# Kernel optimization log

Hardware: AMD Instinct MI355X
Metric: run time of the kernel (lower is better)

The kernel has to match this reference:

```python
import jax, jax.numpy as jnp
import numpy as np

K = 20        # knn neighbors (hardcoded default in get_graph_feature)
EPS = 1e-5    # BatchNorm eps (torch default)


def _bn(x, gamma, beta):
    # training-mode BatchNorm2d: batch stats over (B, N, k) per channel; x: (B, C, N, k)
    mean = jnp.mean(x, axis=(0, 2, 3), keepdims=True)
    var = jnp.var(x, axis=(0, 2, 3), keepdims=True)  # biased, as torch uses for normalization
    return (x - mean) * jax.lax.rsqrt(var + EPS) * gamma[None, :, None, None] + beta[None, :, None, None]


def _graph_feature(x, k):
    # x: (B, D, N) -> (B, 2D, N, k)  [edge features: (neighbor, center)]
    xt = jnp.swapaxes(x, 1, 2)                       # (B, N, D)
    sq = jnp.sum(x * x, axis=1)                      # (B, N)
    inner = jnp.einsum('bnd,bmd->bnm', xt, xt)       # (B, N, N)
    neg_dist = 2.0 * inner - sq[:, :, None] - sq[:, None, :]  # -||xi-xj||^2
    _, idx = jax.lax.top_k(neg_dist, k)              # (B, N, k) nearest neighbors
    feat = jax.vmap(lambda f, i: f[i])(xt, idx)      # (B, N, k, D) gather
    center = jnp.broadcast_to(xt[:, :, None, :], feat.shape)
    g = jnp.concatenate([feat, center], axis=-1)     # (B, N, k, 2D)
    return jnp.transpose(g, (0, 3, 1, 2))            # (B, 2D, N, k)


def _conv1x1(W, x):
    # W: (out, in), x: (B, in, N, k)
    return jnp.einsum('oi,bink->bonk', W, x)


def setup_inputs() -> dict:
    key = jax.random.key(0)
    ks = jax.random.split(key, 16)
    B, D, N = 8, 3, 2048
    emb = 512
    points = jax.random.normal(ks[0], (B, D, N), dtype=jnp.float32)

    def w(k, o, i):
        return jax.random.normal(k, (o, i), dtype=jnp.float32) * (1.0 / np.sqrt(i))

    inp = {
        'points': points,
        'W1': w(ks[1], 64, 6),
        'W2': w(ks[2], 64, 64),
        'W3': w(ks[3], 128, 64),
        'W4': w(ks[4], 256, 128),
        'W5': w(ks[5], emb, 512),
    }
    chans = [64, 64, 128, 256, emb]
    for j, c in enumerate(chans):
        inp[f'g{j+1}'] = 1.0 + 0.1 * jax.random.normal(ks[6 + j], (c,), dtype=jnp.float32)
        inp[f'b{j+1}'] = 0.1 * jax.random.normal(ks[11 + j], (c,), dtype=jnp.float32)
    return inp


def reference(points, W1, W2, W3, W4, W5, g1, b1, g2, b2, g3, b3, g4, b4, g5, b5):
    B, D, N = points.shape
    x = points - jnp.mean(points, axis=2, keepdims=True)   # de-mean (equivariant embedding)
    h = _graph_feature(x, K)                                # (B, 6, N, K)
    h = jax.nn.relu(_bn(_conv1x1(W1, h), g1, b1))
    x1 = jnp.max(h, axis=-1, keepdims=True)                 # (B, 64, N, 1)
    h = jax.nn.relu(_bn(_conv1x1(W2, h), g2, b2))
    x2 = jnp.max(h, axis=-1, keepdims=True)                 # (B, 64, N, 1)
    h = jax.nn.relu(_bn(_conv1x1(W3, h), g3, b3))
    x3 = jnp.max(h, axis=-1, keepdims=True)                 # (B, 128, N, 1)
    h = jax.nn.relu(_bn(_conv1x1(W4, h), g4, b4))
    x4 = jnp.max(h, axis=-1, keepdims=True)                 # (B, 256, N, 1)
    xc = jnp.concatenate([x1, x2, x3, x4], axis=1)          # (B, 512, N, 1)
    out = _bn(_conv1x1(W5, xc), g5, b5).reshape(B, -1, N)   # (B, emb, N)
    return jax.nn.relu(out)
```

## Files before the change

### kernel.cpp

```cpp
#include <hip/hip_runtime.h>

#define BB 8
#define NN 2048
#define KNN 20
#define NPOS (BB*NN)
#define NEDGE (NPOS*KNN)

typedef _Float16 f16x8 __attribute__((ext_vector_type(8)));
typedef float f32x4 __attribute__((ext_vector_type(4)));

union H16 { _Float16 h; unsigned short u; };
__device__ __forceinline__ unsigned short f2h(float f){ H16 x; x.h = (_Float16)f; return x.u; }
__device__ __forceinline__ float h2f(unsigned short u){ H16 x; x.u = u; return (float)x.h; }
__device__ __forceinline__ unsigned fmap(float f){ unsigned u = __float_as_uint(f); return (u & 0x80000000u) ? ~u : (u | 0x80000000u); }
__device__ __forceinline__ float funmap(unsigned m){ return __uint_as_float((m & 0x80000000u) ? (m & 0x7fffffffu) : ~m); }

__global__ __launch_bounds__(256) void k_demean(const float* __restrict__ pts, float* __restrict__ xt){
  int b = blockIdx.x / 3, d = blockIdx.x % 3;
  const float* row = pts + (size_t)(b*3 + d)*NN;
  __shared__ float red[256];
  int t = threadIdx.x;
  float s = 0.f;
  for (int n = t; n < NN; n += 256) s += row[n];
  red[t] = s; __syncthreads();
  for (int w = 128; w > 0; w >>= 1){ if (t < w) red[t] += red[t+w]; __syncthreads(); }
  float mean = red[0] * (1.0f/NN);
  for (int n = t; n < NN; n += 256) xt[(size_t)(b*NN + n)*4 + d] = row[n] - mean;
}

__global__ __launch_bounds__(256) void k_knn(const float* __restrict__ xt, unsigned short* __restrict__ idxo){
  __shared__ float4 xl[NN];
  __shared__ float tv[KNN][256];
  __shared__ unsigned short ti[KNN][256];
  int b = blockIdx.x >> 6;
  int pbase = (blockIdx.x & 63) * 32;
  int t = threadIdx.x;
  const float4* xb = (const float4*)xt + (size_t)b*NN;
  for (int m = t; m < NN; m += 256){
    float4 v = xb[m];
    v.w = v.x*v.x + v.y*v.y + v.z*v.z;
    xl[m] = v;
  }
  __syncthreads();
  int pl = t >> 3, g = t & 7;
  int n = pbase + pl;
  float4 xn = xl[n];
  float sqn = xn.w;
  for (int j = 0; j < 20; ++j){
    int m = g + (j << 3);
    float4 xm = xl[m];
    float nd = 2.f*(xn.x*xm.x + xn.y*xm.y + xn.z*xm.z) - sqn - xm.w;
    tv[j][t] = nd; ti[j][t] = (unsigned short)m;
  }
  float curmin = tv[0][t]; int minslot = 0;
  #pragma unroll
  for (int j = 1; j < 20; ++j){ float v = tv[j][t]; if (v < curmin){ curmin = v; minslot = j; } }
  for (int j = 20; j < 256; ++j){
    int m = g + (j << 3);
    float4 xm = xl[m];
    float nd = 2.f*(xn.x*xm.x + xn.y*xm.y + xn.z*xm.z) - sqn - xm.w;
    if (nd > curmin){
      tv[minslot][t] = nd; ti[minslot][t] = (unsigned short)m;
      curmin = tv[0][t]; minslot = 0;
      #pragma unroll
      for (int u = 1; u < 20; ++u){ float vv = tv[u][t]; if (vv < curmin){ curmin = vv; minslot = u; } }
    }
  }
  __syncthreads();
  for (int s = 4; s; s >>= 1){
    if (g < s){
      int src = t + s;
      for (int jj = 0; jj < 20; ++jj){
        float v = tv[jj][src];
        if (v > curmin){
          unsigned short mi = ti[jj][src];
          tv[minslot][t] = v; ti[minslot][t] = mi;
          curmin = tv[0][t]; minslot = 0;
          #pragma unroll
          for (int u = 1; u < 20; ++u){ float vv = tv[u][t]; if (vv < curmin){ curmin = vv; minslot = u; } }
        }
      }
    }
    __syncthreads();
  }
  if (g == 0){
    unsigned short* op = idxo + (size_t)(b*NN + pbase + pl)*KNN;
    #pragma unroll
    for (int j = 0; j < 20; ++j) op[j] = ti[j][t];
  }
}

__global__ __launch_bounds__(256) void k_conv1(const float* __restrict__ xt, const unsigned short* __restrict__ idx,
    const float* __restrict__ W1, unsigned short* __restrict__ y1){
  __shared__ float Wl[64*6];
  int t = threadIdx.x;
  for (int i = t; i < 384; i += 256) Wl[i] = W1[i];
  __syncthreads();
  int e = blockIdx.x*256 + t;
  int p = e / KNN;
  int b = p >> 11;
  int n = p & (NN-1);
  int nb = idx[e];
  const float4* xb = (const float4*)xt + (size_t)b*NN;
  float4 xnb = xb[nb], xcn = xb[n];
  unsigned short* yo = y1 + (size_t)e*64;
  #pragma unroll
  for (int o = 0; o < 64; o += 8){
    unsigned short pk[8];
    #pragma unroll
    for (int q = 0; q < 8; ++q){
      const float* w = &Wl[(o+q)*6];
      float v = w[0]*xnb.x + w[1]*xnb.y + w[2]*xnb.z + w[3]*xcn.x + w[4]*xcn.y + w[5]*xcn.z;
      pk[q] = f2h(v);
    }
    uint4 u;
    u.x = (unsigned)pk[0] | ((unsigned)pk[1]<<16);
    u.y = (unsigned)pk[2] | ((unsigned)pk[3]<<16);
    u.z = (unsigned)pk[4] | ((unsigned)pk[5]<<16);
    u.w = (unsigned)pk[6] | ((unsigned)pk[7]<<16);
    *reinterpret_cast<uint4*>(yo + o) = u;
  }
}

__global__ __launch_bounds__(256) void k_stats1(const unsigned short* __restrict__ y, float* __restrict__ st){
  int t = threadIdx.x;
  int c = t & 63, ro = t >> 6;
  float s = 0.f, q = 0.f;
  for (int rb = blockIdx.x; rb < NEDGE/4; rb += gridDim.x){
    float v = h2f(y[(size_t)(rb*4 + ro)*64 + c]);
    s += v; q += v*v;
  }
  __shared__ float red[256];
  red[t] = s; __syncthreads();
  if (t < 64){ for (int g = 1; g < 4; ++g) s += red[t + g*64]; }
  __syncthreads(); red[t] = q; __syncthreads();
  if (t < 64){
    for (int g = 1; g < 4; ++g) q += red[t + g*64];
    int shard = blockIdx.x & 63;
    atomicAdd(&st[c*64 + shard], s);
    atomicAdd(&st[64*64 + c*64 + shard], q);
  }
}

__global__ void k_fin(const float* __restrict__ st, const float* __restrict__ gw, const float* __restrict__ bw,
                      float* __restrict__ act, int C, float inv_n){
  int c = threadIdx.x;
  if (c >= C) return;
  float s = 0.f, q = 0.f;
  for (int i = 0; i < 64; ++i){ s += st[c*64 + i]; q += st[(size_t)C*64 + c*64 + i]; }
  float mean = s*inv_n;
  float var = q*inv_n - mean*mean;
  float sc = gw[c] * rsqrtf(var + 1e-5f);
  act[2*c] = sc; act[2*c+1] = bw[c] - mean*sc;
}

__global__ __launch_bounds__(256) void k_max64(const unsigned short* __restrict__ y, const float* __restrict__ actp,
    unsigned short* __restrict__ xc, int xcoff){
  int gidx = blockIdx.x*256 + threadIdx.x;
  int q = gidx >> 5, cp = gidx & 31;
  int c = cp*2;
  float sc0 = actp[2*c],   sh0 = actp[2*c+1];
  float sc1 = actp[2*c+2], sh1 = actp[2*c+3];
  const unsigned* base = reinterpret_cast<const unsigned*>(y + (size_t)q*KNN*64 + c);
  float m0 = 0.f, m1 = 0.f;
  #pragma unroll
  for (int j = 0; j < KNN; ++j){
    unsigned v = base[(size_t)j*32];
    m0 = fmaxf(m0, sc0*h2f((unsigned short)(v & 0xffffu)) + sh0);
    m1 = fmaxf(m1, sc1*h2f((unsigned short)(v >> 16)) + sh1);
  }
  unsigned outv = (unsigned)f2h(m0) | ((unsigned)f2h(m1) << 16);
  *reinterpret_cast<unsigned*>(xc + (size_t)q*512 + xcoff + c) = outv;
}

__device__ __forceinline__ int tix(int row, int col){ return row*64 + (col ^ ((row & 7) << 2)); }

template<int CIN, int COUT, bool ACT, bool MINMAX, bool BGLOBAL, bool SPLITIN>
__global__ __launch_bounds__(256) void k_mfma(
    const unsigned short* __restrict__ inA, const unsigned short* __restrict__ inB,
    const float* __restrict__ W, const float* __restrict__ actp,
    unsigned short* __restrict__ out, size_t slab_stride,
    float* __restrict__ stat, unsigned* __restrict__ mx, unsigned* __restrict__ mn,
    int ntiles){
  constexpr int NKC = CIN/32;
  __shared__ __align__(16) float T[128*64];
  int t = threadIdx.x, lane = t & 63, w = t >> 6, g = lane >> 4, r16 = lane & 15;
  int o0 = blockIdx.y * 64;
  const f16x8 zf = 0;

  f16x8 breg[BGLOBAL ? 1 : NKC][4];
  if constexpr (!BGLOBAL){
    #pragma unroll
    for (int kc = 0; kc < NKC; ++kc)
      #pragma unroll
      for (int n = 0; n < 4; ++n){
        const float* wp = W + (size_t)(o0 + 16*n + r16)*CIN + kc*32 + g*8;
        float4 w0 = *reinterpret_cast<const float4*>(wp);
        float4 w1 = *reinterpret_cast<const float4*>(wp + 4);
        f16x8 bv;
        bv[0]=(_Float16)w0.x; bv[1]=(_Float16)w0.y; bv[2]=(_Float16)w0.z; bv[3]=(_Float16)w0.w;
        bv[4]=(_Float16)w1.x; bv[5]=(_Float16)w1.y; bv[6]=(_Float16)w1.z; bv[7]=(_Float16)w1.w;
        breg[kc][n] = bv;
      }
  }
  f16x8 scl8[ACT ? NKC : 1], shf8[ACT ? NKC : 1];
  if constexpr (ACT){
    #pragma unroll
    for (int kc = 0; kc < NKC; ++kc){
      int ch0 = kc*32 + g*8;
      const float4* apv = reinterpret_cast<const float4*>(actp + 2*ch0);
      float4 q0 = apv[0], q1 = apv[1], q2 = apv[2], q3 = apv[3];
      f16x8 s, h;
      s[0]=(_Float16)q0.x; h[0]=(_Float16)q0.y; s[1]=(_Float16)q0.z; h[1]=(_Float16)q0.w;
      s[2]=(_Float16)q1.x; h[2]=(_Float16)q1.y; s[3]=(_Float16)q1.z; h[3]=(_Float16)q1.w;
      s[4]=(_Float16)q2.x; h[4]=(_Float16)q2.y; s[5]=(_Float16)q2.z; h[5]=(_Float16)q2.w;
      s[6]=(_Float16)q3.x; h[6]=(_Float16)q3.y; s[7]=(_Float16)q3.z; h[7]=(_Float16)q3.w;
      scl8[kc] = s; shf8[kc] = h;
    }
  }
  float sAcc = 0.f, qAcc = 0.f;
  int cst = t & 63, ps = t >> 6;

  for (int tt = blockIdx.x; tt < ntiles; tt += gridDim.x){
    int p0 = tt * 128;
    int prow = p0 + 32*w + r16;
    f32x4 acc[2][4];
    #pragma unroll
    for (int m = 0; m < 2; ++m)
      #pragma unroll
      for (int n = 0; n < 4; ++n) acc[m][n] = 0.f;

    #pragma unroll
    for (int kc = 0; kc < NKC; ++kc){
      f16x8 af[2];
      #pragma unroll
      for (int m = 0; m < 2; ++m){
        const unsigned short* abase; int kloc, stride;
        if constexpr (SPLITIN){ abase = (kc < NKC/2) ? inA : inB; kloc = kc & (NKC/2 - 1); stride = 64; }
        else { abase = inA; kloc = kc; stride = CIN; }
        f16x8 av = *reinterpret_cast<const f16x8*>(abase + (size_t)(prow + 16*m)*stride + kloc*32 + g*8);
        if constexpr (ACT){
          av = av * scl8[kc] + shf8[kc];
          av = __builtin_elementwise_max(av, zf);
        }
        af[m] = av;
      }
      #pragma unroll
      for (int n = 0; n < 4; ++n){
        f16x8 bv;
        if constexpr (BGLOBAL){
          const float* wp = W + (size_t)(o0 + 16*n + r16)*CIN + kc*32 + g*8;
          float4 w0 = *reinterpret_cast<const float4*>(wp);
          float4 w1 = *reinterpret_cast<const float4*>(wp + 4);
          bv[0]=(_Float16)w0.x; bv[1]=(_Float16)w0.y; bv[2]=(_Float16)w0.z; bv[3]=(_Float16)w0.w;
          bv[4]=(_Float16)w1.x; bv[5]=(_Float16)w1.y; bv[6]=(_Float16)w1.z; bv[7]=(_Float16)w1.w;
        } else bv = breg[kc][n];
        acc[0][n] = __builtin_amdgcn_mfma_f32_16x16x32_f16(af[0], bv, acc[0][n], 0, 0, 0);
        acc[1][n] = __builtin_amdgcn_mfma_f32_16x16x32_f16(af[1], bv, acc[1][n], 0, 0, 0);
      }
    }
    __syncthreads();
    #pragma unroll
    for (int m = 0; m < 2; ++m)
      #pragma unroll
      for (int n = 0; n < 4; ++n)
        #pragma unroll
        for (int r = 0; r < 4; ++r)
          T[tix(32*w + 16*m + 4*g + r, 16*n + r16)] = acc[m][n][r];
    __syncthreads();
    #pragma unroll
    for (int r = 0; r < 32; ++r){
      float v = T[tix(32*ps + r, cst)];
      sAcc += v; qAcc += v*v;
    }
    if constexpr (!MINMAX){
      int row = t >> 1, h = t & 1;
      unsigned short* op = out + (size_t)blockIdx.y*slab_stride + ((size_t)p0 + row)*64 + 32*h;
      unsigned pk[16];
      #pragma unroll
      for (int i = 0; i < 8; ++i){
        float4 v = *reinterpret_cast<const float4*>(&T[tix(row, 32*h + 4*i)]);
        pk[2*i]   = (unsigned)f2h(v.x) | ((unsigned)f2h(v.y) << 16);
        pk[2*i+1] = (unsigned)f2h(v.z) | ((unsigned)f2h(v.w) << 16);
      }
      #pragma unroll
      for (int j = 0; j < 4; ++j){
        uint4 u; u.x = pk[4*j]; u.y = pk[4*j+1]; u.z = pk[4*j+2]; u.w = pk[4*j+3];
        *reinterpret_cast<uint4*>(op + 8*j) = u;
      }
    } else {
      int rlo = p0 + 32*ps, rhi = rlo + 32;
      for (int q = rlo/KNN; q*KNN < rhi; ++q){
        int lo = q*KNN > rlo ? q*KNN : rlo;
        int hi = (q*KNN + KNN) < rhi ? (q*KNN + KNN) : rhi;
        float mxv = -1e30f, mnv = 1e30f;
        for (int r = lo; r < hi; ++r){
          float v = T[tix(r - p0, cst)];
          mxv = fmaxf(mxv, v); mnv = fminf(mnv, v);
        }
        atomicMax(&mx[(size_t)q*COUT + o0 + cst], fmap(mxv));
        atomicMin(&mn[(size_t)q*COUT + o0 + cst], fmap(mnv));
      }
    }
  }
  __syncthreads();
  T[ps*64 + cst] = sAcc;
  __syncthreads();
  float stot = 0.f;
  if (t < 64) stot = T[t] + T[64+t] + T[128+t] + T[192+t];
  __syncthreads();
  T[ps*64 + cst] = qAcc;
  __syncthreads();
  if (t < 64){
    float qtot = T[t] + T[64+t] + T[128+t] + T[192+t];
    int shard = blockIdx.x & 63;
    atomicAdd(&stat[(size_t)(o0 + t)*64 + shard], stot);
    atomicAdd(&stat[(size_t)COUT*64 + (size_t)(o0 + t)*64 + shard], qtot);
  }
}

__global__ __launch_bounds__(256) void k_pool4(const unsigned* __restrict__ mx, const unsigned* __restrict__ mn,
    const float* __restrict__ actp, unsigned short* __restrict__ xc){
  int gidx = blockIdx.x*256 + threadIdx.x;
  int q = gidx >> 8, c = gidx & 255;
  float sc = actp[2*c], sh = actp[2*c+1];
  float raw = (sc >= 0.f) ? funmap(mx[gidx]) : funmap(mn[gidx]);
  xc[(size_t)q*512 + 256 + c] = f2h(fmaxf(0.f, sc*raw + sh));
}

__global__ void k_out(const unsigned short* __restrict__ y5, const float* __restrict__ actp, float* __restrict__ out){
  __shared__ float tile[32][33];
  int b = blockIdx.z, n0 = blockIdx.x*32, c0 = blockIdx.y*32;
  int lx = threadIdx.x, ly = threadIdx.y;
  int slab = c0 >> 6, cin = (c0 & 63) + lx;
  float sc = actp[2*(c0+lx)], sh = actp[2*(c0+lx)+1];
  const unsigned short* yb = y5 + (size_t)slab*NPOS*64 + (size_t)(b*NN + n0)*64 + cin;
  for (int yy = ly; yy < 32; yy += 8)
    tile[yy][lx] = fmaxf(0.f, sc*h2f(yb[(size_t)yy*64]) + sh);
  __syncthreads();
  for (int yy = ly; yy < 32; yy += 8)
    out[((size_t)(b*512 + c0 + yy))*NN + n0 + lx] = tile[lx][yy];
}

extern "C" void kernel_launch(void* const* d_in, const int* in_sizes, int n_in,
                              void* d_out, int out_size, void* d_ws, size_t ws_size,
                              hipStream_t stream){
  const float* pts = (const float*)d_in[0];
  const float* W1 = (const float*)d_in[1];
  const float* W2 = (const float*)d_in[2];
  const float* W3 = (const float*)d_in[3];
  const float* W4 = (const float*)d_in[4];
  const float* W5 = (const float*)d_in[5];
  const float* g1 = (const float*)d_in[6];  const float* b1 = (const float*)d_in[7];
  const float* g2 = (const float*)d_in[8];  const float* b2 = (const float*)d_in[9];
  const float* g3 = (const float*)d_in[10]; const float* b3 = (const float*)d_in[11];
  const float* g4 = (const float*)d_in[12]; const float* b4 = (const float*)d_in[13];
  const float* g5 = (const float*)d_in[14]; const float* b5 = (const float*)d_in[15];

  char* ws = (char*)d_ws;
  float*          xt    = (float*)(ws + 0);
  unsigned short* idxu  = (unsigned short*)(ws + 262144);
  float*          stats = (float*)(ws + 917504);
  float*          acts  = (float*)(ws + 1441792);
  unsigned short* y1    = (unsigned short*)(ws + 2097152);
  unsigned short* y3a   = (unsigned short*)(ws + 2097152);
  unsigned short* y5    = (unsigned short*)(ws + 2097152);
  unsigned short* y2    = (unsigned short*)(ws + 44040192);
  unsigned*       mx    = (unsigned*)(ws + 44040192);
  unsigned*       mn    = (unsigned*)(ws + 60817408);
  unsigned short* y3b   = (unsigned short*)(ws + 85983232);
  unsigned short* xc    = (unsigned short*)(ws + 127926272);
  float* out = (float*)d_out;

  float* st1 = stats + 0,  *st2 = stats + 8192, *st3 = stats + 16384, *st4 = stats + 32768, *st5 = stats + 65536;
  float* ac1 = acts + 0,   *ac2 = acts + 128,   *ac3 = acts + 256,    *ac4 = acts + 512,    *ac5 = acts + 1024;
  const size_t y3stride = (size_t)(85983232 - 2097152) / 2;

  hipMemsetAsync(stats, 0, 524288, stream);
  k_demean<<<24, 256, 0, stream>>>(pts, xt);
  k_knn<<<512, 256, 0, stream>>>(xt, idxu);
  k_conv1<<<NEDGE/256, 256, 0, stream>>>(xt, idxu, W1, y1);
  k_stats1<<<256, 256, 0, stream>>>(y1, st1);
  k_fin<<<1, 64, 0, stream>>>(st1, g1, b1, ac1, 64, 1.f/NEDGE);
  k_max64<<<NPOS*32/256, 256, 0, stream>>>(y1, ac1, xc, 0);
  k_mfma<64,64,true,false,false,false><<<dim3(1280,1), 256, 0, stream>>>(
      y1, nullptr, W2, ac1, y2, 0, st2, nullptr, nullptr, 2560);
  k_fin<<<1, 64, 0, stream>>>(st2, g2, b2, ac2, 64, 1.f/NEDGE);
  k_max64<<<NPOS*32/256, 256, 0, stream>>>(y2, ac2, xc, 64);
  k_mfma<64,128,true,false,false,false><<<dim3(640,2), 256, 0, stream>>>(
      y2, nullptr, W3, ac2, y3a, y3stride, st3, nullptr, nullptr, 2560);
  k_fin<<<1, 128, 0, stream>>>(st3, g3, b3, ac3, 128, 1.f/NEDGE);
  k_max64<<<NPOS*32/256, 256, 0, stream>>>(y3a, ac3, xc, 128);
  k_max64<<<NPOS*32/256, 256, 0, stream>>>(y3b, ac3 + 128, xc, 192);
  hipMemsetAsync(mx, 0x00, 16777216, stream);
  hipMemsetAsync(mn, 0xFF, 16777216, stream);
  k_mfma<128,256,true,true,false,true><<<dim3(320,4), 256, 0, stream>>>(
      y3a, y3b, W4, ac3, nullptr, 0, st4, mx, mn, 2560);
  k_fin<<<1, 256, 0, stream>>>(st4, g4, b4, ac4, 256, 1.f/NEDGE);
  k_pool4<<<NPOS, 256, 0, stream>>>(mx, mn, ac4, xc);
  k_mfma<512,512,false,false,true,false><<<dim3(128,8), 256, 0, stream>>>(
      xc, nullptr, W5, nullptr, y5, (size_t)NPOS*64, st5, nullptr, nullptr, 128);
  k_fin<<<1, 512, 0, stream>>>(st5, g5, b5, ac5, 512, 1.f/NPOS);
  k_out<<<dim3(NN/32, 16, BB), dim3(32, 8), 0, stream>>>(y5, ac5, out);
}
```

Measured before the change: 662.0 us.

## Restructure conv layers: per-wave point-aligned MFMA tiles with fused min/max pooling

```diff
diff --git a/kernel.cpp b/kernel.cpp
--- a/kernel.cpp
+++ b/kernel.cpp
@@ -7,13 +7,15 @@
 #define NEDGE (NPOS*KNN)
 
 typedef _Float16 f16x8 __attribute__((ext_vector_type(8)));
+typedef __fp16 fp16x2 __attribute__((ext_vector_type(2)));
 typedef float f32x4 __attribute__((ext_vector_type(4)));
 
 union H16 { _Float16 h; unsigned short u; };
 __device__ __forceinline__ unsigned short f2h(float f){ H16 x; x.h = (_Float16)f; return x.u; }
 __device__ __forceinline__ float h2f(unsigned short u){ H16 x; x.u = u; return (float)x.h; }
-__device__ __forceinline__ unsigned fmap(float f){ unsigned u = __float_as_uint(f); return (u & 0x80000000u) ? ~u : (u | 0x80000000u); }
-__device__ __forceinline__ float funmap(unsigned m){ return __uint_as_float((m & 0x80000000u) ? (m & 0x7fffffffu) : ~m); }
+__device__ __forceinline__ unsigned pkrtz(float a, float b){
+  union { fp16x2 h; unsigned u; } c; c.h = __builtin_amdgcn_cvt_pkrtz(a, b); return c.u;
+}
 
 __global__ __launch_bounds__(256) void k_demean(const float* __restrict__ pts, float* __restrict__ xt){
   int b = blockIdx.x / 3, d = blockIdx.x % 3;
@@ -88,6 +90,17 @@
     #pragma unroll
     for (int j = 0; j < 20; ++j) op[j] = ti[j][t];
   }
+}
+
+__global__ __launch_bounds__(256) void k_wprep(const float* __restrict__ W2, const float* __restrict__ W3,
+    const float* __restrict__ W4, const float* __restrict__ W5, unsigned short* __restrict__ wh){
+  int i = blockIdx.x*256 + threadIdx.x;
+  float v;
+  if (i < 4096) v = W2[i];
+  else if (i < 12288) v = W3[i-4096];
+  else if (i < 45056) v = W4[i-12288];
+  else v = W5[i-45056];
+  wh[i] = f2h(v);
 }
 
 __global__ __launch_bounds__(256) void k_conv1(const float* __restrict__ xt, const unsigned short* __restrict__ idx,
@@ -106,18 +119,16 @@
   unsigned short* yo = y1 + (size_t)e*64;
   #pragma unroll
   for (int o = 0; o < 64; o += 8){
-    unsigned short pk[8];
-    #pragma unroll
-    for (int q = 0; q < 8; ++q){
-      const float* w = &Wl[(o+q)*6];
-      float v = w[0]*xnb.x + w[1]*xnb.y + w[2]*xnb.z + w[3]*xcn.x + w[4]*xcn.y + w[5]*xcn.z;
-      pk[q] = f2h(v);
-    }
-    uint4 u;
-    u.x = (unsigned)pk[0] | ((unsigned)pk[1]<<16);
-    u.y = (unsigned)pk[2] | ((unsigned)pk[3]<<16);
-    u.z = (unsigned)pk[4] | ((unsigned)pk[5]<<16);
-    u.w = (unsigned)pk[6] | ((unsigned)pk[7]<<16);
+    unsigned pk[4];
+    #pragma unroll
+    for (int q = 0; q < 4; ++q){
+      const float* wa = &Wl[(o+2*q)*6];
+      const float* wb = &Wl[(o+2*q+1)*6];
+      float va = wa[0]*xnb.x + wa[1]*xnb.y + wa[2]*xnb.z + wa[3]*xcn.x + wa[4]*xcn.y + wa[5]*xcn.z;
+      float vb = wb[0]*xnb.x + wb[1]*xnb.y + wb[2]*xnb.z + wb[3]*xcn.x + wb[4]*xcn.y + wb[5]*xcn.z;
+      pk[q] = pkrtz(va, vb);
+    }
+    uint4 u; u.x = pk[0]; u.y = pk[1]; u.z = pk[2]; u.w = pk[3];
     *reinterpret_cast<uint4*>(yo + o) = u;
   }
 }
@@ -169,46 +180,25 @@
     m0 = fmaxf(m0, sc0*h2f((unsigned short)(v & 0xffffu)) + sh0);
     m1 = fmaxf(m1, sc1*h2f((unsigned short)(v >> 16)) + sh1);
   }
-  unsigned outv = (unsigned)f2h(m0) | ((unsigned)f2h(m1) << 16);
-  *reinterpret_cast<unsigned*>(xc + (size_t)q*512 + xcoff + c) = outv;
-}
-
-__device__ __forceinline__ int tix(int row, int col){ return row*64 + (col ^ ((row & 7) << 2)); }
-
-template<int CIN, int COUT, bool ACT, bool MINMAX, bool BGLOBAL, bool SPLITIN>
-__global__ __launch_bounds__(256) void k_mfma(
-    const unsigned short* __restrict__ inA, const unsigned short* __restrict__ inB,
-    const float* __restrict__ W, const float* __restrict__ actp,
-    unsigned short* __restrict__ out, size_t slab_stride,
-    float* __restrict__ stat, unsigned* __restrict__ mx, unsigned* __restrict__ mn,
-    int ntiles){
+  *reinterpret_cast<unsigned*>(xc + (size_t)q*512 + xcoff + c) = pkrtz(m0, m1);
+}
+
+template<int CIN, int COUT, bool ACT, bool POOL>
+__global__ __launch_bounds__(256, 4) void k_cstore(
+    const unsigned short* __restrict__ in, const unsigned short* __restrict__ Wh,
+    const float* __restrict__ actp, unsigned short* __restrict__ out, size_t slabStride,
+    float* __restrict__ stat, unsigned* __restrict__ pm, int Cpm, int NT){
   constexpr int NKC = CIN/32;
-  __shared__ __align__(16) float T[128*64];
-  int t = threadIdx.x, lane = t & 63, w = t >> 6, g = lane >> 4, r16 = lane & 15;
+  __shared__ unsigned short Tw[4][32][68];
+  int t = threadIdx.x, lane = t & 63, w = t >> 6;
+  int g = lane >> 4, r16 = lane & 15;
   int o0 = blockIdx.y * 64;
-  const f16x8 zf = 0;
-
-  f16x8 breg[BGLOBAL ? 1 : NKC][4];
-  if constexpr (!BGLOBAL){
-    #pragma unroll
-    for (int kc = 0; kc < NKC; ++kc)
-      #pragma unroll
-      for (int n = 0; n < 4; ++n){
-        const float* wp = W + (size_t)(o0 + 16*n + r16)*CIN + kc*32 + g*8;
-        float4 w0 = *reinterpret_cast<const float4*>(wp);
-        float4 w1 = *reinterpret_cast<const float4*>(wp + 4);
-        f16x8 bv;
-        bv[0]=(_Float16)w0.x; bv[1]=(_Float16)w0.y; bv[2]=(_Float16)w0.z; bv[3]=(_Float16)w0.w;
-        bv[4]=(_Float16)w1.x; bv[5]=(_Float16)w1.y; bv[6]=(_Float16)w1.z; bv[7]=(_Float16)w1.w;
-        breg[kc][n] = bv;
-      }
-  }
+  const f16x8 zf = (f16x8)(_Float16)0.f;
   f16x8 scl8[ACT ? NKC : 1], shf8[ACT ? NKC : 1];
   if constexpr (ACT){
     #pragma unroll
     for (int kc = 0; kc < NKC; ++kc){
-      int ch0 = kc*32 + g*8;
-      const float4* apv = reinterpret_cast<const float4*>(actp + 2*ch0);
+      const float4* apv = reinterpret_cast<const float4*>(actp + 2*(kc*32 + g*8));
       float4 q0 = apv[0], q1 = apv[1], q2 = apv[2], q3 = apv[3];
       f16x8 s, h;
       s[0]=(_Float16)q0.x; h[0]=(_Float16)q0.y; s[1]=(_Float16)q0.z; h[1]=(_Float16)q0.w;
@@ -218,114 +208,206 @@
       scl8[kc] = s; shf8[kc] = h;
     }
   }
-  float sAcc = 0.f, qAcc = 0.f;
-  int cst = t & 63, ps = t >> 6;
-
-  for (int tt = blockIdx.x; tt < ntiles; tt += gridDim.x){
-    int p0 = tt * 128;
-    int prow = p0 + 32*w + r16;
+  float sA[4][4] = {}, qA[4][4] = {};
+  int wid = blockIdx.x*4 + w;
+  for (int tt = wid; tt < NT; tt += gridDim.x*4){
+    int p0 = POOL ? tt*20 : tt*32;
+    int ra = p0 + r16, rb = p0 + 16 + r16;
+    if constexpr (POOL){ ra = min(ra, NEDGE-1); rb = min(rb, NEDGE-1); }
     f32x4 acc[2][4];
     #pragma unroll
     for (int m = 0; m < 2; ++m)
       #pragma unroll
       for (int n = 0; n < 4; ++n) acc[m][n] = 0.f;
-
-    #pragma unroll
+    #pragma unroll 4
     for (int kc = 0; kc < NKC; ++kc){
-      f16x8 af[2];
-      #pragma unroll
-      for (int m = 0; m < 2; ++m){
-        const unsigned short* abase; int kloc, stride;
-        if constexpr (SPLITIN){ abase = (kc < NKC/2) ? inA : inB; kloc = kc & (NKC/2 - 1); stride = 64; }
-        else { abase = inA; kloc = kc; stride = CIN; }
-        f16x8 av = *reinterpret_cast<const f16x8*>(abase + (size_t)(prow + 16*m)*stride + kloc*32 + g*8);
-        if constexpr (ACT){
-          av = av * scl8[kc] + shf8[kc];
-          av = __builtin_elementwise_max(av, zf);
+      f16x8 a0 = *reinterpret_cast<const f16x8*>(in + (size_t)ra*CIN + kc*32 + g*8);
+      f16x8 a1 = *reinterpret_cast<const f16x8*>(in + (size_t)rb*CIN + kc*32 + g*8);
+      if constexpr (ACT){
+        a0 = __builtin_elementwise_max(a0*scl8[kc] + shf8[kc], zf);
+        a1 = __builtin_elementwise_max(a1*scl8[kc] + shf8[kc], zf);
+      }
+      #pragma unroll
+      for (int n = 0; n < 4; ++n){
+        f16x8 bv = *reinterpret_cast<const f16x8*>(Wh + (size_t)(o0 + 16*n + r16)*CIN + kc*32 + g*8);
+        acc[0][n] = __builtin_amdgcn_mfma_f32_16x16x32_f16(bv, a0, acc[0][n], 0, 0, 0);
+        acc[1][n] = __builtin_amdgcn_mfma_f32_16x16x32_f16(bv, a1, acc[1][n], 0, 0, 0);
+      }
+    }
+    #pragma unroll
+    for (int n = 0; n < 4; ++n)
+      #pragma unroll
+      for (int r = 0; r < 4; ++r){
+        float v0 = acc[0][n][r];
+        sA[n][r] += v0; qA[n][r] += v0*v0;
+        if (!POOL || r16 < 4){
+          float v1 = acc[1][n][r];
+          sA[n][r] += v1; qA[n][r] += v1*v1;
         }
-        af[m] = av;
-      }
+      }
+    #pragma unroll
+    for (int m = 0; m < 2; ++m)
       #pragma unroll
       for (int n = 0; n < 4; ++n){
-        f16x8 bv;
-        if constexpr (BGLOBAL){
-          const float* wp = W + (size_t)(o0 + 16*n + r16)*CIN + kc*32 + g*8;
-          float4 w0 = *reinterpret_cast<const float4*>(wp);
-          float4 w1 = *reinterpret_cast<const float4*>(wp + 4);
-          bv[0]=(_Float16)w0.x; bv[1]=(_Float16)w0.y; bv[2]=(_Float16)w0.z; bv[3]=(_Float16)w0.w;
-          bv[4]=(_Float16)w1.x; bv[5]=(_Float16)w1.y; bv[6]=(_Float16)w1.z; bv[7]=(_Float16)w1.w;
-        } else bv = breg[kc][n];
-        acc[0][n] = __builtin_amdgcn_mfma_f32_16x16x32_f16(af[0], bv, acc[0][n], 0, 0, 0);
-        acc[1][n] = __builtin_amdgcn_mfma_f32_16x16x32_f16(af[1], bv, acc[1][n], 0, 0, 0);
-      }
-    }
-    __syncthreads();
+        unsigned u0 = pkrtz(acc[m][n][0], acc[m][n][1]);
+        unsigned u1 = pkrtz(acc[m][n][2], acc[m][n][3]);
+        uint2 d; d.x = u0; d.y = u1;
+        *reinterpret_cast<uint2*>(&Tw[w][16*m + r16][16*n + 4*g]) = d;
+      }
+    int pos = lane >> 1, chh = (lane & 1) * 32;
+    const unsigned short* rp = &Tw[w][pos][chh];
+    uint2 d0 = *reinterpret_cast<const uint2*>(rp);
+    uint2 d1 = *reinterpret_cast<const uint2*>(rp + 4);
+    uint2 d2 = *reinterpret_cast<const uint2*>(rp + 8);
+    uint2 d3 = *reinterpret_cast<const uint2*>(rp + 12);
+    uint2 d4 = *reinterpret_cast<const uint2*>(rp + 16);
+    uint2 d5 = *reinterpret_cast<const uint2*>(rp + 20);
+    uint2 d6 = *reinterpret_cast<const uint2*>(rp + 24);
+    uint2 d7 = *reinterpret_cast<const uint2*>(rp + 28);
+    if (!POOL || (p0 + pos) < NEDGE){
+      uint4* op = reinterpret_cast<uint4*>(out + blockIdx.y*slabStride + ((size_t)(p0 + pos))*64 + chh);
+      op[0] = make_uint4(d0.x, d0.y, d1.x, d1.y);
+      op[1] = make_uint4(d2.x, d2.y, d3.x, d3.y);
+      op[2] = make_uint4(d4.x, d4.y, d5.x, d5.y);
+      op[3] = make_uint4(d6.x, d6.y, d7.x, d7.y);
+    }
+    if constexpr (POOL){
+      float mxv = -1e30f, mnv = 1e30f;
+      #pragma unroll
+      for (int p = 0; p < 20; ++p){
+        float v = h2f(Tw[w][p][lane]);
+        mxv = fmaxf(mxv, v); mnv = fminf(mnv, v);
+      }
+      pm[(size_t)tt*Cpm + blockIdx.y*64 + lane] = pkrtz(mnv, mxv);
+    }
+  }
+  #pragma unroll
+  for (int n = 0; n < 4; ++n)
+    #pragma unroll
+    for (int r = 0; r < 4; ++r){
+      float s = sA[n][r], q = qA[n][r];
+      #pragma unroll
+      for (int d = 1; d < 16; d <<= 1){ s += __shfl_xor(s, d); q += __shfl_xor(q, d); }
+      sA[n][r] = s; qA[n][r] = q;
+    }
+  if (r16 == 0){
+    int shard = wid & 63;
+    #pragma unroll
+    for (int n = 0; n < 4; ++n)
+      #pragma unroll
+      for (int r = 0; r < 4; ++r){
+        int ch = o0 + 16*n + 4*g + r;
+        atomicAdd(&stat[(size_t)ch*64 + shard], sA[n][r]);
+        atomicAdd(&stat[(size_t)(COUT + ch)*64 + shard], qA[n][r]);
+      }
+  }
+}
+
+__global__ __launch_bounds__(256, 4) void k_conv4(
+    const unsigned short* __restrict__ inA, const unsigned short* __restrict__ inB,
+    const unsigned short* __restrict__ Wh, const float* __restrict__ actp,
+    float* __restrict__ stat, unsigned* __restrict__ pm){
+  int t = threadIdx.x, lane = t & 63, w = t >> 6;
+  int g = lane >> 4, r16 = lane & 15;
+  int o0 = blockIdx.y * 64;
+  const f16x8 zf = (f16x8)(_Float16)0.f;
+  f16x8 scl8[4], shf8[4];
+  #pragma unroll
+  for (int kc = 0; kc < 4; ++kc){
+    const float4* apv = reinterpret_cast<const float4*>(actp + 2*(kc*32 + g*8));
+    float4 q0 = apv[0], q1 = apv[1], q2 = apv[2], q3 = apv[3];
+    f16x8 s, h;
+    s[0]=(_Float16)q0.x; h[0]=(_Float16)q0.y; s[1]=(_Float16)q0.z; h[1]=(_Float16)q0.w;
+    s[2]=(_Float16)q1.x; h[2]=(_Float16)q1.y; s[3]=(_Float16)q1.z; h[3]=(_Float16)q1.w;
+    s[4]=(_Float16)q2.x; h[4]=(_Float16)q2.y; s[5]=(_Float16)q2.z; h[5]=(_Float16)q2.w;
+    s[6]=(_Float16)q3.x; h[6]=(_Float16)q3.y; s[7]=(_Float16)q3.z; h[7]=(_Float16)q3.w;
+    scl8[kc] = s; shf8[kc] = h;
+  }
+  float s4[4] = {}, q4[4] = {};
+  int wid = blockIdx.x*4 + w;
+  for (int q = wid; q < NPOS; q += gridDim.x*4){
+    int p0 = q*20;
+    int ra = min(p0 + r16, NEDGE-1), rb = min(p0 + 16 + r16, NEDGE-1);
+    f32x4 acc[2][4];
     #pragma unroll
     for (int m = 0; m < 2; ++m)
       #pragma unroll
+      for (int n = 0; n < 4; ++n) acc[m][n] = 0.f;
+    #pragma unroll
+    for (int kc = 0; kc < 4; ++kc){
+      const unsigned short* ab = (kc < 2) ? inA : inB;
+      int kl = kc & 1;
+      f16x8 a0 = *reinterpret_cast<const f16x8*>(ab + (size_t)ra*64 + kl*32 + g*8);
+      f16x8 a1 = *reinterpret_cast<const f16x8*>(ab + (size_t)rb*64 + kl*32 + g*8);
+      a0 = __builtin_elementwise_max(a0*scl8[kc] + shf8[kc], zf);
+      a1 = __builtin_elementwise_max(a1*scl8[kc] + shf8[kc], zf);
+      #pragma unroll
+      for (int n = 0; n < 4; ++n){
+        f16x8 bv = *reinterpret_cast<const f16x8*>(Wh + (size_t)(o0 + 16*n + r16)*128 + kc*32 + g*8);
+        acc[0][n] = __builtin_amdgcn_mfma_f32_16x16x32_f16(a0, bv, acc[0][n], 0, 0, 0);
+        acc[1][n] = __builtin_amdgcn_mfma_f32_16x16x32_f16(a1, bv, acc[1][n], 0, 0, 0);
+      }
+    }
+    #pragma unroll
+    for (int n = 0; n < 4; ++n){
+      #pragma unroll
+      for (int r = 0; r < 4; ++r){ float v = acc[0][n][r]; s4[n] += v; q4[n] += v*v; }
+      if (g == 0){
+        #pragma unroll
+        for (int r = 0; r < 4; ++r){ float v = acc[1][n][r]; s4[n] += v; q4[n] += v*v; }
+      }
+    }
+    float mxv[4], mnv[4];
+    #pragma unroll
+    for (int n = 0; n < 4; ++n){
+      float mx = fmaxf(fmaxf(acc[0][n][0], acc[0][n][1]), fmaxf(acc[0][n][2], acc[0][n][3]));
+      float mn = fminf(fminf(acc[0][n][0], acc[0][n][1]), fminf(acc[0][n][2], acc[0][n][3]));
+      if (g == 0){
+        mx = fmaxf(mx, fmaxf(fmaxf(acc[1][n][0], acc[1][n][1]), fmaxf(acc[1][n][2], acc[1][n][3])));
+        mn = fminf(mn, fminf(fminf(acc[1][n][0], acc[1][n][1]), fminf(acc[1][n][2], acc[1][n][3])));
+      }
+      mxv[n] = mx; mnv[n] = mn;
+    }
+    #pragma unroll
+    for (int n = 0; n < 4; ++n){
+      mxv[n] = fmaxf(mxv[n], __shfl_xor(mxv[n], 16));
+      mnv[n] = fminf(mnv[n], __shfl_xor(mnv[n], 16));
+      mxv[n] = fmaxf(mxv[n], __shfl_xor(mxv[n], 32));
+      mnv[n] = fminf(mnv[n], __shfl_xor(mnv[n], 32));
+    }
+    if (lane < 16){
+      #pragma unroll
       for (int n = 0; n < 4; ++n)
-        #pragma unroll
-        for (int r = 0; r < 4; ++r)
-          T[tix(32*w + 16*m + 4*g + r, 16*n + r16)] = acc[m][n][r];
-    __syncthreads();
-    #pragma unroll
-    for (int r = 0; r < 32; ++r){
-      float v = T[tix(32*ps + r, cst)];
-      sAcc += v; qAcc += v*v;
-    }
-    if constexpr (!MINMAX){
-      int row = t >> 1, h = t & 1;
-      unsigned short* op = out + (size_t)blockIdx.y*slab_stride + ((size_t)p0 + row)*64 + 32*h;
-      unsigned pk[16];
-      #pragma unroll
-      for (int i = 0; i < 8; ++i){
-        float4 v = *reinterpret_cast<const float4*>(&T[tix(row, 32*h + 4*i)]);
-        pk[2*i]   = (unsigned)f2h(v.x) | ((unsigned)f2h(v.y) << 16);
-        pk[2*i+1] = (unsigned)f2h(v.z) | ((unsigned)f2h(v.w) << 16);
-      }
-      #pragma unroll
-      for (int j = 0; j < 4; ++j){
-        uint4 u; u.x = pk[4*j]; u.y = pk[4*j+1]; u.z = pk[4*j+2]; u.w = pk[4*j+3];
-        *reinterpret_cast<uint4*>(op + 8*j) = u;
-      }
-    } else {
-      int rlo = p0 + 32*ps, rhi = rlo + 32;
-      for (int q = rlo/KNN; q*KNN < rhi; ++q){
-        int lo = q*KNN > rlo ? q*KNN : rlo;
-        int hi = (q*KNN + KNN) < rhi ? (q*KNN + KNN) : rhi;
-        float mxv = -1e30f, mnv = 1e30f;
-        for (int r = lo; r < hi; ++r){
-          float v = T[tix(r - p0, cst)];
-          mxv = fmaxf(mxv, v); mnv = fminf(mnv, v);
-        }
-        atomicMax(&mx[(size_t)q*COUT + o0 + cst], fmap(mxv));
-        atomicMin(&mn[(size_t)q*COUT + o0 + cst], fmap(mnv));
-      }
-    }
-  }
-  __syncthreads();
-  T[ps*64 + cst] = sAcc;
-  __syncthreads();
-  float stot = 0.f;
-  if (t < 64) stot = T[t] + T[64+t] + T[128+t] + T[192+t];
-  __syncthreads();
-  T[ps*64 + cst] = qAcc;
-  __syncthreads();
-  if (t < 64){
-    float qtot = T[t] + T[64+t] + T[128+t] + T[192+t];
-    int shard = blockIdx.x & 63;
-    atomicAdd(&stat[(size_t)(o0 + t)*64 + shard], stot);
-    atomicAdd(&stat[(size_t)COUT*64 + (size_t)(o0 + t)*64 + shard], qtot);
-  }
-}
-
-__global__ __launch_bounds__(256) void k_pool4(const unsigned* __restrict__ mx, const unsigned* __restrict__ mn,
-    const float* __restrict__ actp, unsigned short* __restrict__ xc){
-  int gidx = blockIdx.x*256 + threadIdx.x;
-  int q = gidx >> 8, c = gidx & 255;
+        pm[(size_t)q*256 + o0 + 16*n + lane] = pkrtz(mnv[n], mxv[n]);
+    }
+  }
+  #pragma unroll
+  for (int n = 0; n < 4; ++n){
+    s4[n] += __shfl_xor(s4[n], 16); q4[n] += __shfl_xor(q4[n], 16);
+    s4[n] += __shfl_xor(s4[n], 32); q4[n] += __shfl_xor(q4[n], 32);
+  }
+  if (lane < 16){
+    int shard = wid & 63;
+    #pragma unroll
+    for (int n = 0; n < 4; ++n){
+      int ch = o0 + 16*n + lane;
+      atomicAdd(&stat[(size_t)ch*64 + shard], s4[n]);
+      atomicAdd(&stat[(size_t)(256 + ch)*64 + shard], q4[n]);
+    }
+  }
+}
+
+template<int C>
+__global__ __launch_bounds__(256) void k_poolfin(const unsigned* __restrict__ pm, const float* __restrict__ actp,
+    unsigned short* __restrict__ xc, int coff){
+  int gi = blockIdx.x*256 + threadIdx.x;
+  int q = gi / C, c = gi % C;
+  unsigned v = pm[gi];
+  float mnv = h2f((unsigned short)(v & 0xffffu));
+  float mxv = h2f((unsigned short)(v >> 16));
   float sc = actp[2*c], sh = actp[2*c+1];
-  float raw = (sc >= 0.f) ? funmap(mx[gidx]) : funmap(mn[gidx]);
-  xc[(size_t)q*512 + 256 + c] = f2h(fmaxf(0.f, sc*raw + sh));
+  float raw = (sc >= 0.f) ? mxv : mnv;
+  xc[(size_t)q*512 + coff + c] = f2h(fmaxf(0.f, sc*raw + sh));
 }
 
 __global__ void k_out(const unsigned short* __restrict__ y5, const float* __restrict__ actp, float* __restrict__ out){
@@ -362,44 +444,48 @@
   unsigned short* idxu  = (unsigned short*)(ws + 262144);
   float*          stats = (float*)(ws + 917504);
   float*          acts  = (float*)(ws + 1441792);
+  unsigned short* wh    = (unsigned short*)(ws + 1449984);
   unsigned short* y1    = (unsigned short*)(ws + 2097152);
   unsigned short* y3a   = (unsigned short*)(ws + 2097152);
   unsigned short* y5    = (unsigned short*)(ws + 2097152);
   unsigned short* y2    = (unsigned short*)(ws + 44040192);
-  unsigned*       mx    = (unsigned*)(ws + 44040192);
-  unsigned*       mn    = (unsigned*)(ws + 60817408);
+  unsigned*       pm4   = (unsigned*)(ws + 44040192);
+  unsigned*       pm2   = (unsigned*)(ws + 85983232);
   unsigned short* y3b   = (unsigned short*)(ws + 85983232);
   unsigned short* xc    = (unsigned short*)(ws + 127926272);
+  unsigned*       pm3   = (unsigned*)(ws + 144703488);
   float* out = (float*)d_out;
+
+  unsigned short* w2h = wh;
+  unsigned short* w3h = wh + 4096;
+  unsigned short* w4h = wh + 12288;
+  unsigned short* w5h = wh + 45056;
 
   float* st1 = stats + 0,  *st2 = stats + 8192, *st3 = stats + 16384, *st4 = stats + 32768, *st5 = stats + 65536;
   float* ac1 = acts + 0,   *ac2 = acts + 128,   *ac3 = acts + 256,    *ac4 = acts + 512,    *ac5 = acts + 1024;
   const size_t y3stride = (size_t)(85983232 - 2097152) / 2;
 
   hipMemsetAsync(stats, 0, 524288, stream);
+  k_wprep<<<1200, 256, 0, stream>>>(W2, W3, W4, W5, wh);
   k_demean<<<24, 256, 0, stream>>>(pts, xt);
   k_knn<<<512, 256, 0, stream>>>(xt, idxu);
   k_conv1<<<NEDGE/256, 256, 0, stream>>>(xt, idxu, W1, y1);
   k_stats1<<<256, 256, 0, stream>>>(y1, st1);
   k_fin<<<1, 64, 0, stream>>>(st1, g1, b1, ac1, 64, 1.f/NEDGE);
   k_max64<<<NPOS*32/256, 256, 0, stream>>>(y1, ac1, xc, 0);
-  k_mfma<64,64,true,false,false,false><<<dim3(1280,1), 256, 0, stream>>>(
-      y1, nullptr, W2, ac1, y2, 0, st2, nullptr, nullptr, 2560);
+  k_cstore<64,64,true,true><<<dim3(1024,1), 256, 0, stream>>>(
+      y1, w2h, ac1, y2, 0, st2, pm2, 64, NEDGE/20);
   k_fin<<<1, 64, 0, stream>>>(st2, g2, b2, ac2, 64, 1.f/NEDGE);
-  k_max64<<<NPOS*32/256, 256, 0, stream>>>(y2, ac2, xc, 64);
-  k_mfma<64,128,true,false,false,false><<<dim3(640,2), 256, 0, stream>>>(
-      y2, nullptr, W3, ac2, y3a, y3stride, st3, nullptr, nullptr, 2560);
+  k_poolfin<64><<<NPOS*64/256, 256, 0, stream>>>(pm2, ac2, xc, 64);
+  k_cstore<64,128,true,true><<<dim3(1024,2), 256, 0, stream>>>(
+      y2, w3h, ac2, y3a, y3stride, st3, pm3, 128, NEDGE/20);
   k_fin<<<1, 128, 0, stream>>>(st3, g3, b3, ac3, 128, 1.f/NEDGE);
-  k_max64<<<NPOS*32/256, 256, 0, stream>>>(y3a, ac3, xc, 128);
-  k_max64<<<NPOS*32/256, 256, 0, stream>>>(y3b, ac3 + 128, xc, 192);
-  hipMemsetAsync(mx, 0x00, 16777216, stream);
-  hipMemsetAsync(mn, 0xFF, 16777216, stream);
-  k_mfma<128,256,true,true,false,true><<<dim3(320,4), 256, 0, stream>>>(
-      y3a, y3b, W4, ac3, nullptr, 0, st4, mx, mn, 2560);
+  k_poolfin<128><<<NPOS*128/256, 256, 0, stream>>>(pm3, ac3, xc, 128);
+  k_conv4<<<dim3(1024,4), 256, 0, stream>>>(y3a, y3b, w4h, ac3, st4, pm4);
   k_fin<<<1, 256, 0, stream>>>(st4, g4, b4, ac4, 256, 1.f/NEDGE);
-  k_pool4<<<NPOS, 256, 0, stream>>>(mx, mn, ac4, xc);
-  k_mfma<512,512,false,false,true,false><<<dim3(128,8), 256, 0, stream>>>(
-      xc, nullptr, W5, nullptr, y5, (size_t)NPOS*64, st5, nullptr, nullptr, 128);
+  k_poolfin<256><<<NPOS*256/256, 256, 0, stream>>>(pm4, ac4, xc, 256);
+  k_cstore<512,512,false,false><<<dim3(128,8), 256, 0, stream>>>(
+      xc, w5h, nullptr, y5, (size_t)NPOS*64, st5, nullptr, 0, NPOS/32);
   k_fin<<<1, 512, 0, stream>>>(st5, g5, b5, ac5, 512, 1.f/NPOS);
   k_out<<<dim3(NN/32, 16, BB), dim3(32, 8), 0, stream>>>(y5, ac5, out);
 }
```

After: 1.106 ms. 1.67x slower.
